# Kernel optimization log

Hardware: AMD Instinct MI355X
Metric: run time of the kernel (lower is better)

## Reference

```python
import jax, jax.numpy as jnp
import numpy as np
from jax.scipy.special import logsumexp

K = 15          # top-k
N = 4096        # n candidates
BS = 128        # batch size
EPS = 0.1       # entropic regularizer epsilon
MAX_ITER = 200  # Sinkhorn iterations
RANK = 5        # rank of pseudoinverse init
SMALL = 1e-20


def _build_weights():
    """Rank-5 pseudoinverse of Sinkhorn constraint matrix A (as in __init__).
    A maps (f in R^n, g in R^k) -> (f_i + g_c) over rows r = i*(k+1)+c (g_k := 0).
    A^T A = [[(k+1) I_n, J_{n x k}], [J_{k x n}, n I_k]] in closed form."""
    k1 = K + 1
    p = N + K
    G = np.zeros((p, p), dtype=np.float64)
    G[:N, :N] = (k1) * np.eye(N)
    G[:N, N:] = 1.0
    G[N:, :N] = 1.0
    G[N:, N:] = N * np.eye(K)
    w, V = np.linalg.eigh(G)
    idx = np.argsort(w)[-RANK:]
    s = np.sqrt(w[idx])
    V = V[:, idx]                                  # (p, RANK)
    # U = A @ V / s without materializing A (1GB dense):
    vf = V[:N]                                     # (N, RANK)
    vg = np.concatenate([V[N:], np.zeros((1, RANK))], axis=0)  # (k1, RANK)
    U = (vf[:, None, :] + vg[None, :, :]).reshape(N * k1, RANK) / s
    weight1 = (V / s).astype(np.float32)           # (N+K, RANK) = V diag(1/s)
    weight2 = U.T.astype(np.float32)               # (RANK, N*(K+1)) = U^T
    return jnp.asarray(weight1), jnp.asarray(weight2)


def setup_inputs() -> dict:
    key = jax.random.key(0)
    scores = jax.random.normal(key, (BS, N), dtype=jnp.float32)
    tau = jnp.ones((1,), jnp.float32) * 0.1
    weight1, weight2 = _build_weights()
    return {"scores": scores, "tau": tau, "weight1": weight1, "weight2": weight2}


def _sinkhorn(C, mu, nu, Gamma0, weight1, weight2):
    bs, n, k1 = C.shape
    # least-squares warm start for potentials f, g
    b = (C + EPS * jnp.log(Gamma0)).reshape(bs, -1)          # (bs, n*k1)
    x = jnp.einsum('bm,rm->br', b, weight2)                  # (bs, RANK)
    x = jnp.einsum('br,pr->bp', x, weight1)                  # (bs, n+k)
    f = x[:, :n, None]                                       # (bs, n, 1)
    g = jnp.concatenate([x[:, n:], jnp.zeros((bs, 1), C.dtype)], axis=-1)[:, None, :]  # (bs,1,k1)
    elog_mu = EPS * jnp.log(mu)                              # (1, n, 1)
    elog_nu = EPS * jnp.log(nu)                              # (1, 1, k1)

    def step(carry, _):
        f, g = carry
        f = -EPS * logsumexp(-(C - g) / EPS, axis=-1, keepdims=True) + elog_mu
        g = -EPS * logsumexp(-(C - f) / EPS, axis=-2, keepdims=True) + elog_nu
        return (f, g), None

    (f, g), _ = jax.lax.scan(step, (f, g), None, length=MAX_ITER)
    return jnp.exp((-C + f + g) / EPS)


def reference(scores, tau, weight1, weight2):
    bs, n = scores.shape
    k = K
    s = scores[:, :, None]                                   # (bs, n, 1)
    sd = jax.lax.stop_gradient(s)
    max_s = jnp.max(sd)
    min_s = jnp.min(jnp.where(jnp.isneginf(sd), jnp.inf, sd))
    filled = min_s - (max_s - min_s)
    s = jnp.where(jnp.isneginf(s), filled, s)
    anchors = jnp.arange(k, -1, -1, dtype=s.dtype).reshape(1, 1, k + 1)
    C = (s - anchors) ** 2
    C = C / jax.lax.stop_gradient(C.max())
    mu = jnp.full((1, n, 1), 1.0 / n, dtype=s.dtype)
    nu = jnp.concatenate([jnp.full((k,), 1.0 / n), jnp.array([(n - k) / n])]).astype(s.dtype).reshape(1, 1, k + 1)
    # warm-start transport plan Gamma0 from (detached) hard top-k
    topk_val = jax.lax.top_k(jax.lax.stop_gradient(s[..., 0]), k)[0]      # (bs, k)
    Gamma0 = jax.nn.sigmoid(-jnp.abs(topk_val[:, None, :] - s) / tau)     # (bs, n, k)
    Gamma0 = Gamma0 + SMALL
    Gamma0 = Gamma0 / Gamma0.sum(-2, keepdims=True) / n
    Gamma0_last = jnp.clip(1.0 / n - Gamma0.sum(-1, keepdims=True), SMALL, 1.0 - SMALL)
    Gamma0 = jnp.concatenate([Gamma0, Gamma0_last], axis=-1)              # (bs, n, k+1)
    Gamma = _sinkhorn(C, mu, nu, Gamma0, weight1, weight2)
    A = Gamma[:, :, :k] * n
    return A, jnp.linalg.norm(Gamma - Gamma0)
```

## Files before the change

kernel.cpp:

```cpp
#include <hip/hip_runtime.h>
#include <math.h>

#define KK 15
#define K1 16
#define NN 4096
#define BSZ 128
#define NT 512
#define RPT 8
#define NPAIR 4
#define NW 8
#define EPSI 0.1f
#define SMALLC 1e-20f
#define NITER 200
#define W2STRIDE 65536
#define OUT_A_ELEMS (BSZ * NN * KK)
#define TS 20
#define CONV_REL 5e-7f

typedef __attribute__((ext_vector_type(2))) float f2;
typedef __attribute__((ext_vector_type(2))) unsigned u2v;
__device__ __forceinline__ f2 pk_fma(f2 a, f2 b, f2 c){
  return __builtin_elementwise_fma(a, b, c);
}

__device__ __forceinline__ unsigned enc_f32(float f){
  unsigned u = __float_as_uint(f);
  return (u & 0x80000000u) ? ~u : (u | 0x80000000u);
}
__device__ __forceinline__ float dec_f32(unsigned e){
  unsigned u = (e & 0x80000000u) ? (e ^ 0x80000000u) : ~e;
  return __uint_as_float(u);
}


template<int CTRL>
__device__ __forceinline__ float dpp_movf(float x){
  return __uint_as_float((unsigned)__builtin_amdgcn_update_dpp(
      (int)0, (int)__float_as_uint(x), CTRL, 0xF, 0xF, true));
}

__device__ __forceinline__ float bcast_lane0(float x){
  return __uint_as_float((unsigned)__builtin_amdgcn_readlane(
      (int)__float_as_uint(x), 0));
}

__device__ __forceinline__ float xsum16(float r){
#if __has_builtin(__builtin_amdgcn_permlane16_swap)
  u2v s = __builtin_amdgcn_permlane16_swap(__float_as_uint(r), __float_as_uint(r), false, false);
  return __uint_as_float(s.x) + __uint_as_float(s.y);
#else
  return r + __shfl_xor(r, 16);
#endif
}
__device__ __forceinline__ float xsum32(float r){
#if __has_builtin(__builtin_amdgcn_permlane32_swap)
  u2v s = __builtin_amdgcn_permlane32_swap(__float_as_uint(r), __float_as_uint(r), false, false);
  return __uint_as_float(s.x) + __uint_as_float(s.y);
#else
  return r + __shfl_xor(r, 32);
#endif
}

__device__ __forceinline__ float sum16_all(float v){
  v += dpp_movf<0x128>(v);
  v += dpp_movf<0x124>(v);
  v += dpp_movf<0x4E>(v);
  v += dpp_movf<0xB1>(v);
  return v;
}

__device__ __forceinline__ int fold_col(int lane){
  int l = lane & 15;
  return ((l & 1) << 3) | ((l & 2) << 1) | ((l & 8) >> 2) | ((l & 4) >> 2);
}

__device__ __forceinline__ float wave_fold16(const float p[K1], int lane){
  float a[8];
  {
    const bool hi = (lane & 1) != 0;
    #pragma unroll
    for (int j = 0; j < 8; ++j){
      float send = hi ? p[j] : p[j + 8];
      float keep = hi ? p[j + 8] : p[j];
      a[j] = keep + dpp_movf<0xB1>(send);
    }
  }
  float bq[4];
  {
    const bool hi = (lane & 2) != 0;
    #pragma unroll
    for (int j = 0; j < 4; ++j){
      float send = hi ? a[j] : a[j + 4];
      float keep = hi ? a[j + 4] : a[j];
      bq[j] = keep + dpp_movf<0x4E>(send);
    }
  }
  float cq[2];
  {
    const bool hi = (lane & 8) != 0;
    float s0 = hi ? bq[0] : bq[2];
    float s1 = hi ? bq[1] : bq[3];
    float k0 = hi ? bq[2] : bq[0];
    float k1 = hi ? bq[3] : bq[1];
    cq[0] = k0 + dpp_movf<0x128>(s0);
    cq[1] = k1 + dpp_movf<0x128>(s1);
  }
  float r;
  {
    const bool hi = (lane & 4) != 0;
    float send = hi ? cq[0] : cq[1];
    float keep = hi ? cq[1] : cq[0];
    r = keep + __shfl_xor(send, 4);
  }
  r = xsum16(r);
  r = xsum32(r);
  return r;
}

__device__ __forceinline__ void block_fold16(const float p[K1], float* wb, float* tb,
                                             int lane, int wv, int tid){
  float r = wave_fold16(p, lane);
  if (lane < 16) wb[wv * K1 + fold_col(lane)] = r;
  __syncthreads();
  if (tid < 16){
    float t = 0.0f;
    #pragma unroll
    for (int q = 0; q < NW; ++q) t += wb[q * K1 + tid];
    tb[tid] = t;
  }
  __syncthreads();
}

__global__ __launch_bounds__(NT, 2) void k_main(
    const float* __restrict__ scores, const float* __restrict__ taup,
    const float* __restrict__ w1, const float* __restrict__ w2,
    float* __restrict__ out, unsigned* __restrict__ ws){
  const int b = blockIdx.x;
  const int tid = threadIdx.x;
  const int lane = tid & 63;
  const int wv = tid >> 6;

  __shared__ float scratch[NN];
  __shared__ float tk[KK];
  __shared__ int tki[KK];
  __shared__ __align__(16) float cbuf[K1];
  __shared__ float wbuf[NW * K1];
  __shared__ __align__(16) float xbuf[K1];
  __shared__ __align__(16) float wbufT[2][K1 * TS];
  __shared__ float rv[NW];
  __shared__ int ri[NW];
  __shared__ float rmn[NW];
  __shared__ unsigned sng[NW];
  __shared__ float statb[4];

  float raw[RPT];
  #pragma unroll
  for (int j = 0; j < RPT; ++j) raw[j] = scores[(size_t)b * NN + tid + NT * j];

  {
    float mx = -INFINITY, mn = INFINITY; unsigned neg = 0u;
    #pragma unroll
    for (int j = 0; j < RPT; ++j){
      float v = raw[j];
      mx = fmaxf(mx, v);
      if (v == -INFINITY) neg = 1u; else mn = fminf(mn, v);
    }
    #pragma unroll
    for (int off = 32; off; off >>= 1){
      mx = fmaxf(mx, __shfl_xor(mx, off));
      mn = fminf(mn, __shfl_xor(mn, off));
      neg |= (unsigned)__shfl_xor((int)neg, off);
    }
    if (lane == 0){ rv[wv] = mx; rmn[wv] = mn; sng[wv] = neg; }
    __syncthreads();
    if (tid == 0){
      for (int q = 1; q < NW; ++q){
        mx = fmaxf(mx, rv[q]); mn = fminf(mn, rmn[q]); neg |= sng[q];
      }
      atomicMax(&ws[0], enc_f32(mx));
      atomicMin(&ws[5], enc_f32(mn));
      if (neg) atomicOr(&ws[1], 1u);
      __threadfence();
      atomicAdd(&ws[3], 1u);
      while (__hip_atomic_load(&ws[3], __ATOMIC_ACQUIRE, __HIP_MEMORY_SCOPE_AGENT) < (unsigned)BSZ)
        __builtin_amdgcn_s_sleep(2);
      statb[0] = dec_f32(__hip_atomic_load(&ws[0], __ATOMIC_RELAXED, __HIP_MEMORY_SCOPE_AGENT));
      statb[1] = dec_f32(__hip_atomic_load(&ws[5], __ATOMIC_RELAXED, __HIP_MEMORY_SCOPE_AGENT));
      statb[2] = __hip_atomic_load(&ws[1], __ATOMIC_RELAXED, __HIP_MEMORY_SCOPE_AGENT) ? 1.0f : 0.0f;
    }
    __syncthreads();
  }

  const float smax = statb[0];
  const float smin_raw = statb[1];
  const bool has_neg = statb[2] != 0.0f;
  const float filled = smin_raw - (smax - smin_raw);
  const float smin_eff = has_neg ? filled : smin_raw;
  const float cmax = fmaxf(fmaxf(smin_eff * smin_eff, smax * smax),
                           fmaxf((smin_eff - 15.0f) * (smin_eff - 15.0f),
                                 (smax - 15.0f) * (smax - 15.0f)));
  const float cinv = 1.0f / cmax;
  const float tauv = taup[0];
  const float invtau = 1.0f / tauv;
  const float inv_n = 1.0f / (float)NN;

  #pragma unroll
  for (int j = 0; j < RPT; ++j){
    float v = raw[j]; if (v == -INFINITY) v = filled;
    scratch[tid + NT * j] = v;
  }
  __syncthreads();

  for (int t = 0; t < KK; ++t){
    float bv = -INFINITY; int bi = NN;
    #pragma unroll
    for (int j = 0; j < RPT; ++j){
      int i = tid + NT * j;
      float v = scratch[i];
      if (v > bv){ bv = v; bi = i; }
    }
    #pragma unroll
    for (int off = 32; off; off >>= 1){
      float ov = __shfl_xor(bv, off);
      int oi = __shfl_xor(bi, off);
      if (ov > bv || (ov == bv && oi < bi)){ bv = ov; bi = oi; }
    }
    if (lane == 0){ rv[wv] = bv; ri[wv] = bi; }
    __syncthreads();
    {
      float mv = -INFINITY; int mi = NN;
      if (tid < NW){ mv = rv[tid]; mi = ri[tid]; }
      #pragma unroll
      for (int off = 4; off; off >>= 1){
        float ov = __shfl_xor(mv, off);
        int oi = __shfl_xor(mi, off);
        if (ov > mv || (ov == mv && oi < mi)){ mv = ov; mi = oi; }
      }
      if (tid == 0){
        tk[t] = mv; tki[t] = mi;
        scratch[mi] = -INFINITY;
      }
    }
    __syncthreads();
  }
  if (tid < KK) scratch[tki[tid]] = tk[tid];
  __syncthreads();

  {
    float p[K1];
    float tkr[KK];
    #pragma unroll
    for (int c = 0; c < KK; ++c) tkr[c] = tk[c];
    #pragma unroll
    for (int c = 0; c < K1; ++c) p[c] = 0.0f;
    #pragma unroll
    for (int j = 0; j < RPT; ++j){
      float si = scratch[tid + NT * j];
      #pragma unroll
      for (int c = 0; c < KK; ++c){
        float z = fabsf(tkr[c] - si) * invtau;
        float raw1 = __builtin_amdgcn_rcpf(1.0f + __expf(z)) + SMALLC;
        p[c] += raw1;
      }
    }
    block_fold16(p, wbuf, cbuf, lane, wv, tid);
  }

  float colinv_n[KK];
  {
    float p[K1];
    float tkr[KK];
    #pragma unroll
    for (int c = 0; c < KK; ++c){
      tkr[c] = tk[c];
      colinv_n[c] = (1.0f / cbuf[c]) * inv_n;
    }
    #pragma unroll
    for (int c = 0; c < K1; ++c) p[c] = 0.0f;
    #pragma unroll
    for (int j = 0; j < RPT; ++j){
      int i = tid + NT * j;
      float si = scratch[i];
      float bb[K1];
      float rowpart = 0.0f;
      #pragma unroll
      for (int c = 0; c < KK; ++c){
        float d = si - (float)(KK - c);
        float Cc = d * d * cinv;
        float z = fabsf(tkr[c] - si) * invtau;
        float raw1 = __builtin_amdgcn_rcpf(1.0f + __expf(z)) + SMALLC;
        float g0 = raw1 * colinv_n[c];
        rowpart += g0;
        bb[c] = Cc + EPSI * __logf(g0);
      }
      {
        float Cc = si * si * cinv;
        float g0l = fminf(fmaxf(inv_n - rowpart, SMALLC), 1.0f - SMALLC);
        bb[KK] = Cc + EPSI * __logf(g0l);
      }
      #pragma unroll
      for (int r = 0; r < 5; ++r){
        const float4* wp = (const float4*)(w2 + (size_t)r * W2STRIDE + (size_t)i * K1);
        float4 a0 = wp[0], a1 = wp[1], a2 = wp[2], a3 = wp[3];
        float acc = p[r];
        acc += bb[0] * a0.x + bb[1] * a0.y + bb[2] * a0.z + bb[3] * a0.w;
        acc += bb[4] * a1.x + bb[5] * a1.y + bb[6] * a1.z + bb[7] * a1.w;
        acc += bb[8] * a2.x + bb[9] * a2.y + bb[10] * a2.z + bb[11] * a2.w;
        acc += bb[12] * a3.x + bb[13] * a3.y + bb[14] * a3.z + bb[15] * a3.w;
        p[r] = acc;
      }
    }
    block_fold16(p, wbuf, xbuf, lane, wv, tid);
  }

  float vt[K1];
  {
    float xv[5];
    #pragma unroll
    for (int r = 0; r < 5; ++r) xv[r] = xbuf[r];
    #pragma unroll
    for (int c = 0; c < KK; ++c){
      float g = 0.0f;
      #pragma unroll
      for (int r = 0; r < 5; ++r) g += xv[r] * w1[(size_t)(NN + c) * 5 + r];
      float Bc = expf(-10.0f * cinv * (float)((KK - c) * (KK - c)));
      vt[c] = Bc * expf(g * 10.0f);
    }
    vt[KK] = 1.0f;
  }

  f2 x2[NPAIR];
  #pragma unroll
  for (int q = 0; q < NPAIR; ++q){
    float s0 = scratch[tid + NT * (2 * q)];
    float s1 = scratch[tid + NT * (2 * q + 1)];
    x2[q].x = expf(s0 * (-20.0f * cinv));
    x2[q].y = expf(s1 * (-20.0f * cinv));
  }
  f2 xp[NPAIR][K1];
  #pragma unroll
  for (int q = 0; q < NPAIR; ++q){
    xp[q][0].x = 1.0f; xp[q][0].y = 1.0f;
    xp[q][1] = x2[q];
    #pragma unroll
    for (int c = 2; c < K1; ++c) xp[q][c] = xp[q][c - 1] * x2[q];
  }

  f2 t2[NPAIR];
  const float nmul = ((lane & 15) < KK) ? 1.0f : 4081.0f;
  float pv2 = 0.0f, pv1 = 0.0f;
  int pcnt = -1;
  #pragma unroll 1
  for (int it = 0; it < NITER; ++it){
    const int ph = it & 1;
    #pragma unroll
    for (int q = 0; q < NPAIR; ++q){
      f2 h; h.x = vt[KK]; h.y = vt[KK];
      #pragma unroll
      for (int c = KK - 1; c >= 0; --c){
        f2 vc; vc.x = vt[c]; vc.y = vt[c];
        h = pk_fma(h, x2[q], vc);
      }
      t2[q].x = __builtin_amdgcn_rcpf(h.x);
      t2[q].y = __builtin_amdgcn_rcpf(h.y);
    }
    float p[K1];
    #pragma unroll
    for (int c = 0; c < K1; ++c){
      f2 s = t2[0] * xp[0][c];
      #pragma unroll
      for (int q = 1; q < NPAIR; ++q) s = pk_fma(t2[q], xp[q][c], s);
      p[c] = s.x + s.y;
    }
    float r = wave_fold16(p, lane);
    if (lane < 16) wbufT[ph][fold_col(lane) * TS + wv] = r;
    __syncthreads();
    float md = -1.0f;
    float wout = 0.0f;
    if (lane < 16){
      const float* wp = &wbufT[ph][lane * TS];
      float4 a4 = *(const float4*)wp;
      float4 b4 = *(const float4*)(wp + 4);
      float t = ((a4.x + a4.y) + (a4.z + a4.w)) + ((b4.x + b4.y) + (b4.z + b4.w));
      float wnew = nmul * __builtin_amdgcn_rcpf(t);
      md = fabsf(wnew - pv1) - CONV_REL * pv1;
      wout = wnew;
    }
    if (pcnt >= 1){
      float r1 = 0.0f, r2 = 0.0f;
      if (lane < 16){
        float winv = __builtin_amdgcn_rcpf(wout);
        r1 = (pv1 - pv2) * winv;
        r2 = (wout - pv1) * winv;
      }
      float s12 = sum16_all(r1 * r2);
      float s11 = sum16_all(r1 * r1);
      float s12b = bcast_lane0(s12);
      float s11b = bcast_lane0(s11);
      int anymove = __any((lane < 16) && (fabsf(r2) > 4.0f * CONV_REL));
      float fac = s12b * __builtin_amdgcn_rcpf(s11b - s12b);
      float acc = wout * (1.0f + r2 * fac);
      int okbr = (lane < 16) ? (acc > 0.1f * wout && acc < 10.0f * wout) : 1;
      int allbr = __all(okbr);
      if ((s12b > 0.0f) && (s12b < 0.97f * s11b) && anymove && allbr){
        if (lane < 16) wout = acc;
        pcnt = -1;
      }
    }
    pcnt++;
    pv2 = pv1; pv1 = wout;
    int conv = __all(md <= 0.0f);
    #pragma unroll
    for (int c = 0; c < K1; ++c)
      vt[c] = __uint_as_float((unsigned)__builtin_amdgcn_readlane(
                  (int)__float_as_uint(wout), c));
    if (conv) break;
  }

  float nrm = 0.0f;
  {
    float tkr[KK];
    #pragma unroll
    for (int c = 0; c < KK; ++c) tkr[c] = tk[c];
    #pragma unroll
    for (int q = 0; q < NPAIR; ++q){
      #pragma unroll
      for (int half = 0; half < 2; ++half){
        int i = tid + NT * (2 * q + half);
        float si = scratch[i];
        float tin = (half ? t2[q].y : t2[q].x) * inv_n;
        float rowpart = 0.0f;
        float gamv[KK];
        float gaml;
        #pragma unroll
        for (int c = 0; c < KK; ++c){
          float xc = half ? xp[q][c].y : xp[q][c].x;
          float gam = (tin * xc) * vt[c];
          float z = fabsf(tkr[c] - si) * invtau;
          float raw1 = __builtin_amdgcn_rcpf(1.0f + __expf(z)) + SMALLC;
          float g0 = raw1 * colinv_n[c];
          rowpart += g0;
          float d = gam - g0;
          nrm += d * d;
          gamv[c] = gam * (float)NN;
        }
        {
          float xc = half ? xp[q][KK].y : xp[q][KK].x;
          gaml = (tin * xc) * vt[KK];
          float g0l = fminf(fmaxf(inv_n - rowpart, SMALLC), 1.0f - SMALLC);
          float d = gaml - g0l;
          nrm += d * d;
        }
        float* op = out + (size_t)(b * NN + i) * KK;
        #pragma unroll
        for (int c = 0; c < KK; ++c) op[c] = gamv[c];
      }
    }
  }
  #pragma unroll
  for (int off = 32; off; off >>= 1) nrm += __shfl_xor(nrm, off);
  if (lane == 0) rv[wv] = nrm;
  __syncthreads();
  if (tid == 0){
    float t = 0.0f;
    for (int q = 0; q < NW; ++q) t += rv[q];
    atomicAdd(reinterpret_cast<float*>(ws) + 2, t);
    __threadfence();
    unsigned prev = atomicAdd(&ws[4], 1u);
    if (prev == (unsigned)(BSZ - 1)){
      float n2 = __hip_atomic_load(reinterpret_cast<float*>(ws) + 2,
                                   __ATOMIC_RELAXED, __HIP_MEMORY_SCOPE_AGENT);
      out[OUT_A_ELEMS] = sqrtf(n2);
    }
  }
}

extern "C" void kernel_launch(void* const* d_in, const int* in_sizes, int n_in,
                              void* d_out, int out_size, void* d_ws, size_t ws_size,
                              hipStream_t stream){
  const float* scores = (const float*)d_in[0];
  const float* tau    = (const float*)d_in[1];
  const float* w1     = (const float*)d_in[2];
  const float* w2     = (const float*)d_in[3];
  float* out = (float*)d_out;
  unsigned* ws = (unsigned*)d_ws;

  hipMemsetAsync(ws, 0x00, 20, stream);
  hipMemsetAsync((char*)ws + 20, 0xFF, 4, stream);

  k_main<<<BSZ, NT, 0, stream>>>(scores, tau, w1, w2, out, ws);
}
```

Baseline: 150.5 us.

## Add Newton warm-up phase for Sinkhorn column scalings before fixed-point loop

```diff
diff --git a/kernel.cpp b/kernel.cpp
--- a/kernel.cpp
+++ b/kernel.cpp
@@ -12,6 +12,7 @@
 #define EPSI 0.1f
 #define SMALLC 1e-20f
 #define NITER 200
+#define MAXNEWT 7
 #define W2STRIDE 65536
 #define OUT_A_ELEMS (BSZ * NN * KK)
 #define TS 20
@@ -39,9 +40,9 @@
       (int)0, (int)__float_as_uint(x), CTRL, 0xF, 0xF, true));
 }
 
-__device__ __forceinline__ float bcast_lane0(float x){
+__device__ __forceinline__ float readlane_f(float x, int sl){
   return __uint_as_float((unsigned)__builtin_amdgcn_readlane(
-      (int)__float_as_uint(x), 0));
+      (int)__float_as_uint(x), sl));
 }
 
 __device__ __forceinline__ float xsum16(float r){
@@ -61,14 +62,6 @@
 #endif
 }
 
-__device__ __forceinline__ float sum16_all(float v){
-  v += dpp_movf<0x128>(v);
-  v += dpp_movf<0x124>(v);
-  v += dpp_movf<0x4E>(v);
-  v += dpp_movf<0xB1>(v);
-  return v;
-}
-
 __device__ __forceinline__ int fold_col(int lane){
   int l = lane & 15;
   return ((l & 1) << 3) | ((l & 2) << 1) | ((l & 8) >> 2) | ((l & 4) >> 2);
@@ -129,6 +122,45 @@
     tb[tid] = t;
   }
   __syncthreads();
+}
+
+__device__ __forceinline__ void row_sweep(const float vt[K1], const f2 x2[NPAIR],
+                                          f2 t2[NPAIR]){
+  #pragma unroll
+  for (int q = 0; q < NPAIR; ++q){
+    f2 h; h.x = vt[KK]; h.y = vt[KK];
+    #pragma unroll
+    for (int c = KK - 1; c >= 0; --c){
+      f2 vc; vc.x = vt[c]; vc.y = vt[c];
+      h = pk_fma(h, x2[q], vc);
+    }
+    t2[q].x = __builtin_amdgcn_rcpf(h.x);
+    t2[q].y = __builtin_amdgcn_rcpf(h.y);
+  }
+}
+
+__device__ __forceinline__ float chain_fold(const f2 seed[NPAIR], const f2 x2[NPAIR],
+                                            int lane){
+  f2 acc[K1];
+  #pragma unroll
+  for (int q = 0; q < NPAIR; ++q){
+    f2 u = seed[q];
+    #pragma unroll
+    for (int c = 0; c < K1; ++c){
+      if (q == 0) acc[c] = u; else acc[c] += u;
+      if (c < KK) u = u * x2[q];
+    }
+  }
+  float p[K1];
+  #pragma unroll
+  for (int c = 0; c < K1; ++c) p[c] = acc[c].x + acc[c].y;
+  return wave_fold16(p, lane);
+}
+
+__device__ __forceinline__ float sum8_col(const float* base){
+  float4 a4 = *(const float4*)base;
+  float4 b4 = *(const float4*)(base + 4);
+  return ((a4.x + a4.y) + (a4.z + a4.w)) + ((b4.x + b4.y) + (b4.z + b4.w));
 }
 
 __global__ __launch_bounds__(NT, 2) void k_main(
@@ -147,6 +179,8 @@
   __shared__ float wbuf[NW * K1];
   __shared__ __align__(16) float xbuf[K1];
   __shared__ __align__(16) float wbufT[2][K1 * TS];
+  __shared__ __align__(16) float mbufB[K1 * TS];
+  __shared__ float mlds[NW][32];
   __shared__ float rv[NW];
   __shared__ int ri[NW];
   __shared__ float rmn[NW];
@@ -347,73 +381,118 @@
   }
 
   f2 t2[NPAIR];
-  const float nmul = ((lane & 15) < KK) ? 1.0f : 4081.0f;
-  float pv2 = 0.0f, pv1 = 0.0f;
-  int pcnt = -1;
+  const int l15 = lane & 15;
+  const float nmul = (l15 < KK) ? 1.0f : 4081.0f;
+  const float nmul_inv = (l15 < KK) ? 1.0f : (1.0f / 4081.0f);
+  float pv1 = 0.0f;
+  #pragma unroll
+  for (int c = 0; c < K1; ++c) pv1 = (l15 == c) ? vt[c] : pv1;
+
+  f2 xp8[NPAIR];
+  #pragma unroll
+  for (int q = 0; q < NPAIR; ++q) xp8[q] = xp[q][8];
+
+  #pragma unroll 1
+  for (int nit = 0; nit < MAXNEWT; ++nit){
+    row_sweep(vt, x2, t2);
+    float rS = chain_fold(t2, x2, lane);
+    f2 sA[NPAIR], sB[NPAIR];
+    #pragma unroll
+    for (int q = 0; q < NPAIR; ++q){
+      sA[q] = t2[q] * t2[q];
+      f2 w8 = t2[q] * xp8[q];
+      sB[q] = w8 * w8;
+    }
+    float rA = chain_fold(sA, x2, lane);
+    float rB = chain_fold(sB, x2, lane);
+    if (lane < 16){
+      wbufT[0][fold_col(lane) * TS + wv] = rS;
+      wbufT[1][fold_col(lane) * TS + wv] = rA;
+      mbufB[fold_col(lane) * TS + wv] = rB;
+    }
+    __syncthreads();
+    float wnew = 0.0f, relr = -1.0f;
+    if (lane < 16){
+      float S  = sum8_col(&wbufT[0][lane * TS]);
+      float MA = sum8_col(&wbufT[1][lane * TS]);
+      float MB = sum8_col(&mbufB[lane * TS]);
+      wnew = nmul * __builtin_amdgcn_rcpf(S);
+      relr = fabsf(wnew - pv1) - CONV_REL * pv1;
+      mlds[wv][lane] = MA;
+      mlds[wv][lane + 16] = MB;
+    }
+    int done = __all(relr <= 0.0f);
+    if (done){
+      if (lane < 16) pv1 = wnew;
+      #pragma unroll
+      for (int c = 0; c < K1; ++c) vt[c] = readlane_f(wnew, c);
+      __syncthreads();
+      break;
+    }
+    float Mld[K1];
+    #pragma unroll
+    for (int d = 0; d < K1; ++d) Mld[d] = mlds[wv][l15 + d];
+    float A[K1], bbv;
+    {
+      float rinv = __builtin_amdgcn_rcpf(pv1);
+      float fFsc = wnew * wnew * nmul_inv;
+      #pragma unroll
+      for (int d = 0; d < K1; ++d){
+        float Jld = fFsc * Mld[d] * vt[d] * rinv;
+        A[d] = ((l15 == d) ? 1.0f : 0.0f) - Jld;
+      }
+      bbv = wnew * rinv - 1.0f;
+      if (l15 == KK){
+        #pragma unroll
+        for (int d = 0; d < K1; ++d) A[d] = (d == KK) ? 1.0f : 0.0f;
+        bbv = 0.0f;
+      }
+    }
+    #pragma unroll
+    for (int p = 0; p < K1; ++p){
+      float App = readlane_f(A[p], p);
+      float pinv = __builtin_amdgcn_rcpf(App);
+      float fac = (l15 == p) ? 0.0f : A[p] * pinv;
+      #pragma unroll
+      for (int d = p; d < K1; ++d){
+        float Apd = readlane_f(A[d], p);
+        A[d] = fmaf(-fac, Apd, A[d]);
+      }
+      float Apb = readlane_f(bbv, p);
+      bbv = fmaf(-fac, Apb, bbv);
+    }
+    float diag = 1.0f;
+    #pragma unroll
+    for (int d = 0; d < K1; ++d) diag = (l15 == d) ? A[d] : diag;
+    float eta = bbv * __builtin_amdgcn_rcpf(diag);
+    float wcand = pv1 * (1.0f + eta);
+    int okl = (lane < 16) ? ((fabsf(eta) < 0.69f) && (wcand > 0.0f)) : 1;
+    int ok = __all(okl);
+    float wout = ok ? wcand : wnew;
+    if (lane < 16) pv1 = wout;
+    #pragma unroll
+    for (int c = 0; c < K1; ++c) vt[c] = readlane_f(wout, c);
+    __syncthreads();
+  }
+
   #pragma unroll 1
   for (int it = 0; it < NITER; ++it){
     const int ph = it & 1;
-    #pragma unroll
-    for (int q = 0; q < NPAIR; ++q){
-      f2 h; h.x = vt[KK]; h.y = vt[KK];
-      #pragma unroll
-      for (int c = KK - 1; c >= 0; --c){
-        f2 vc; vc.x = vt[c]; vc.y = vt[c];
-        h = pk_fma(h, x2[q], vc);
-      }
-      t2[q].x = __builtin_amdgcn_rcpf(h.x);
-      t2[q].y = __builtin_amdgcn_rcpf(h.y);
-    }
-    float p[K1];
-    #pragma unroll
-    for (int c = 0; c < K1; ++c){
-      f2 s = t2[0] * xp[0][c];
-      #pragma unroll
-      for (int q = 1; q < NPAIR; ++q) s = pk_fma(t2[q], xp[q][c], s);
-      p[c] = s.x + s.y;
-    }
-    float r = wave_fold16(p, lane);
+    row_sweep(vt, x2, t2);
+    float r = chain_fold(t2, x2, lane);
     if (lane < 16) wbufT[ph][fold_col(lane) * TS + wv] = r;
     __syncthreads();
     float md = -1.0f;
     float wout = 0.0f;
     if (lane < 16){
-      const float* wp = &wbufT[ph][lane * TS];
-      float4 a4 = *(const float4*)wp;
-      float4 b4 = *(const float4*)(wp + 4);
-      float t = ((a4.x + a4.y) + (a4.z + a4.w)) + ((b4.x + b4.y) + (b4.z + b4.w));
-      float wnew = nmul * __builtin_amdgcn_rcpf(t);
-      md = fabsf(wnew - pv1) - CONV_REL * pv1;
-      wout = wnew;
-    }
-    if (pcnt >= 1){
-      float r1 = 0.0f, r2 = 0.0f;
-      if (lane < 16){
-        float winv = __builtin_amdgcn_rcpf(wout);
-        r1 = (pv1 - pv2) * winv;
-        r2 = (wout - pv1) * winv;
-      }
-      float s12 = sum16_all(r1 * r2);
-      float s11 = sum16_all(r1 * r1);
-      float s12b = bcast_lane0(s12);
-      float s11b = bcast_lane0(s11);
-      int anymove = __any((lane < 16) && (fabsf(r2) > 4.0f * CONV_REL));
-      float fac = s12b * __builtin_amdgcn_rcpf(s11b - s12b);
-      float acc = wout * (1.0f + r2 * fac);
-      int okbr = (lane < 16) ? (acc > 0.1f * wout && acc < 10.0f * wout) : 1;
-      int allbr = __all(okbr);
-      if ((s12b > 0.0f) && (s12b < 0.97f * s11b) && anymove && allbr){
-        if (lane < 16) wout = acc;
-        pcnt = -1;
-      }
-    }
-    pcnt++;
-    pv2 = pv1; pv1 = wout;
+      float t = sum8_col(&wbufT[ph][lane * TS]);
+      wout = nmul * __builtin_amdgcn_rcpf(t);
+      md = fabsf(wout - pv1) - CONV_REL * pv1;
+      pv1 = wout;
+    }
     int conv = __all(md <= 0.0f);
     #pragma unroll
-    for (int c = 0; c < K1; ++c)
-      vt[c] = __uint_as_float((unsigned)__builtin_amdgcn_readlane(
-                  (int)__float_as_uint(wout), c));
+    for (int c = 0; c < K1; ++c) vt[c] = readlane_f(wout, c);
     if (conv) break;
   }
 
```

Result: slower. 158.9 us (+5.6%).
